# Kernel tuning notes

Hardware: AMD Instinct MI355X
Metric: run time of the kernel (lower is better)

Reference implementation:

```python
import jax, jax.numpy as jnp
import numpy as np
import math

B, T = 32768, 34
VOCAB = 14
SQRT_HD = math.sqrt(3.0)

def _pos_flat_index():
    # flatten (source, index) pairs into indices of a [14,3] table:
    # rows 0-9 = digit spiral enc, row 10 = z10_enc, rows 11-13 = special_enc
    flat = []
    for p in range(34):
        if p < 10:
            flat.append(p)
        elif p == 10:
            flat.append(11 + 0)
        elif p < 21:
            flat.append(p - 11)
        elif p == 21:
            flat.append(11 + 1)
        elif p < 33:
            z = p - 22
            flat.append(z if z < 10 else 10)
        else:
            flat.append(11 + 2)
    return np.array(flat, dtype=np.int32)

POS_FLAT = _pos_flat_index()

def setup_inputs() -> dict:
    key = jax.random.key(0)
    ks = jax.random.split(key, 12)
    r = lambda k, s: jax.random.normal(k, s, dtype=jnp.float32)
    return {
        'idx': jax.random.randint(ks[0], (B, T), 0, VOCAB, dtype=jnp.int64),
        'tok_emb': r(ks[1], (14, 3)),
        'pos_params': r(ks[2], (4,)),
        'z10_enc': r(ks[3], (1, 3)),
        'special_enc': r(ks[4], (3, 3)),
        'wq': r(ks[5], (3, 6)), 'wk': r(ks[6], (3, 6)), 'wv': r(ks[7], (3, 6)),
        'wo': r(ks[8], (6, 6)),
        'ln1_g': jnp.ones(6), 'ln1_b': jnp.zeros(6),
        'ln2_g': jnp.ones(6), 'ln2_b': jnp.zeros(6),
        'lnf_g': jnp.ones(6), 'lnf_b': jnp.zeros(6),
        'ffn_w1': r(ks[9], (6, 2)), 'ffn_b1': jnp.zeros(2),
        'ffn_w2': r(ks[10], (2, 6)), 'ffn_b2': jnp.zeros(6),
        'head_w': r(ks[11], (6, 3)),
    }

def _ln(x, g, b):
    mu = x.mean(-1, keepdims=True)
    var = ((x - mu) ** 2).mean(-1, keepdims=True)
    return (x - mu) * jax.lax.rsqrt(var + 1e-5) * g + b

def _forward(idx, tok_emb, pos_params, z10_enc, special_enc, wq, wk, wv, wo,
             ln1_g, ln1_b, ln2_g, ln2_b, lnf_g, lnf_b,
             ffn_w1, ffn_b1, ffn_w2, ffn_b2, head_w):
    amp, phase, slope, offset = pos_params[0], pos_params[1], pos_params[2], pos_params[3]
    i = jnp.arange(10, dtype=jnp.float32)
    ang = 2.0 * math.pi * i / 10.0 + phase
    digit = jnp.stack([amp * jnp.cos(ang), amp * jnp.sin(ang), slope * i + offset], -1)  # [10,3]
    table = jnp.concatenate([digit, z10_enc, special_enc], 0)  # [14,3]
    Tn = idx.shape[1]
    pos = table[POS_FLAT][:Tn]  # [T,3]
    tok = tok_emb[idx]  # [B,T,3]
    x = jnp.concatenate([tok, jnp.broadcast_to(pos, tok.shape)], -1)  # [B,T,6]
    h = _ln(x, ln1_g, ln1_b)
    h_tok, h_pos = h[..., :3], h[..., 3:]
    Bn = idx.shape[0]
    q = (h_pos @ wq).reshape(Bn, Tn, 2, 3)
    k = (h_pos @ wk).reshape(Bn, Tn, 2, 3)
    v = (h_tok @ wv).reshape(Bn, Tn, 2, 3)
    attn = jnp.einsum('bqhd,bkhd->bhqk', q, k) / SQRT_HD
    mask = jnp.tril(jnp.ones((Tn, Tn), bool))
    attn = jax.nn.softmax(jnp.where(mask, attn, -jnp.inf), axis=-1)
    o = jnp.einsum('bhqk,bkhd->bqhd', attn, v).reshape(Bn, Tn, 6)
    x = x + o @ wo
    h2 = _ln(x, ln2_g, ln2_b)
    x = x + (jax.nn.gelu(h2 @ ffn_w1 + ffn_b1, approximate=False) @ ffn_w2 + ffn_b2)
    x = _ln(x, lnf_g, lnf_b)
    return (x @ head_w) @ tok_emb.T  # [B,T,14]

def reference(idx, tok_emb, pos_params, z10_enc, special_enc, wq, wk, wv, wo,
              ln1_g, ln1_b, ln2_g, ln2_b, lnf_g, lnf_b,
              ffn_w1, ffn_b1, ffn_w2, ffn_b2, head_w):
    return _forward(idx, tok_emb, pos_params, z10_enc, special_enc, wq, wk, wv, wo,
                    ln1_g, ln1_b, ln2_g, ln2_b, lnf_g, lnf_b,
                    ffn_w1, ffn_b1, ffn_w2, ffn_b2, head_w)
```

## Files before the change

kernel.cpp:

```cpp
#include <hip/hip_runtime.h>
#include <math.h>

#define BT    34
#define TPR   17
#define RPB   15
#define BLOCK 256

typedef float v2f __attribute__((ext_vector_type(2)));
typedef float v4f __attribute__((ext_vector_type(4)));

#define QSCALE 0.83294037332470f

#if __has_builtin(__builtin_amdgcn_exp2f)
#define EXP2(x) __builtin_amdgcn_exp2f(x)
#else
#define EXP2(x) exp2f(x)
#endif

__device__ __forceinline__ void ln6n(const v2f* x, v2f* o) {
  v2f mu = (x[0]+x[1]+x[2]+x[3]+x[4]+x[5]) * (1.0f/6.0f);
  v2f v = (v2f){0.f, 0.f};
  #pragma unroll
  for (int c = 0; c < 6; ++c) { v2f d = x[c]-mu; v += d*d; }
  v2f inv = (v2f){ rsqrtf(v.x*(1.0f/6.0f) + 1e-5f),
                   rsqrtf(v.y*(1.0f/6.0f) + 1e-5f) };
  #pragma unroll
  for (int c = 0; c < 6; ++c) o[c] = (x[c]-mu)*inv;
}

__global__ __launch_bounds__(BLOCK, 6)
void addtrans_kernel(const int* __restrict__ idx,
                     const float* __restrict__ tok_emb,
                     const float* __restrict__ pos_params,
                     const float* __restrict__ z10_enc,
                     const float* __restrict__ special_enc,
                     const float* __restrict__ wq,
                     const float* __restrict__ wk,
                     const float* __restrict__ wv,
                     const float* __restrict__ wo,
                     const float* __restrict__ ln1_g, const float* __restrict__ ln1_b,
                     const float* __restrict__ ln2_g, const float* __restrict__ ln2_b,
                     const float* __restrict__ lnf_g, const float* __restrict__ lnf_b,
                     const float* __restrict__ ffn_w1, const float* __restrict__ ffn_b1,
                     const float* __restrict__ ffn_w2, const float* __restrict__ ffn_b2,
                     const float* __restrict__ head_w,
                     float* __restrict__ out, int B)
{
  __shared__ __align__(16) float s_mem[RPB*BT*12 + 180];
  __shared__ float s_te[42];
  __shared__ float s_pos[BT*3];
  __shared__ float s_wqf[18], s_wkf[18], s_wvf[18];
  __shared__ float s_qb[6], s_kb[6], s_vb[6];
  __shared__ float s_wo[36];
  __shared__ float s_w1f[12], s_fb1f[2];
  __shared__ float s_w2[12], s_fb2[6];
  __shared__ float s_hwf[18], s_yb[3];

  const int tid = threadIdx.x;
  const int b0  = blockIdx.x * RPB;

  if (tid < 42) s_te[tid] = tok_emb[tid];
  if (tid < 18) {
    const int r = tid / 6;
    s_wqf[tid] = wq[tid] * ln1_g[3+r];
    s_wkf[tid] = wk[tid] * ln1_g[3+r];
    s_wvf[tid] = wv[tid] * ln1_g[r];
    s_hwf[tid] = head_w[tid] * lnf_g[tid/3];
  }
  if (tid < 36) s_wo[tid] = wo[tid];
  if (tid < 12) { s_w1f[tid] = ffn_w1[tid] * ln2_g[tid>>1]; s_w2[tid] = ffn_w2[tid]; }
  if (tid < 6)  {
    s_qb[tid] = ln1_b[3]*wq[tid] + ln1_b[4]*wq[6+tid] + ln1_b[5]*wq[12+tid];
    s_kb[tid] = ln1_b[3]*wk[tid] + ln1_b[4]*wk[6+tid] + ln1_b[5]*wk[12+tid];
    s_vb[tid] = ln1_b[0]*wv[tid] + ln1_b[1]*wv[6+tid] + ln1_b[2]*wv[12+tid];
    s_fb2[tid] = ffn_b2[tid];
  }
  if (tid < 3) {
    float a = 0.f;
    #pragma unroll
    for (int c = 0; c < 6; ++c) a += lnf_b[c]*head_w[c*3+tid];
    s_yb[tid] = a;
  }
  if (tid < 2) {
    float a = ffn_b1[tid];
    #pragma unroll
    for (int d = 0; d < 6; ++d) a += ln2_b[d]*ffn_w1[d*2+tid];
    s_fb1f[tid] = a;
  }
  if (tid < BT) {
    int p = tid, f;
    if (p < 10) f = p;
    else if (p == 10) f = 11;
    else if (p < 21) f = p - 11;
    else if (p == 21) f = 12;
    else if (p < 33) { int z = p - 22; f = (z < 10) ? z : 10; }
    else f = 13;
    float e0, e1, e2;
    if (f < 10) {
      float amp = pos_params[0], ph = pos_params[1], sl = pos_params[2], of = pos_params[3];
      float ang = 0.62831853071795864769f * (float)f + ph;
      e0 = amp * cosf(ang); e1 = amp * sinf(ang); e2 = sl * (float)f + of;
    } else if (f == 10) { e0 = z10_enc[0]; e1 = z10_enc[1]; e2 = z10_enc[2]; }
    else { int u = f - 11; e0 = special_enc[u*3]; e1 = special_enc[u*3+1]; e2 = special_enc[u*3+2]; }
    s_pos[tid*3+0] = e0; s_pos[tid*3+1] = e1; s_pos[tid*3+2] = e2;
  }
  __syncthreads();

  const int row = tid % RPB;
  const int j   = tid / RPB;
  const int b   = b0 + row;
  const bool active = (j < TPR) && (b < B);

  v2f qpA[3], qpB[3];
  v2f x6[6];

  if (active) {
    const int tA = j, tB = j + TPR;
    const int vA = idx[b*BT + tA];
    const int vB = idx[b*BT + tB];
    #pragma unroll
    for (int c = 0; c < 3; ++c) {
      x6[c]   = (v2f){ s_te[vA*3+c],  s_te[vB*3+c]  };
      x6[3+c] = (v2f){ s_pos[tA*3+c], s_pos[tB*3+c] };
    }
    v2f h[6];
    ln6n(x6, h);
    v2f q6[6], k6[6], v6[6];
    #pragma unroll
    for (int c = 0; c < 6; ++c) {
      q6[c] = (v2f){s_qb[c], s_qb[c]} + h[3]*s_wqf[c] + h[4]*s_wqf[6+c] + h[5]*s_wqf[12+c];
      k6[c] = (v2f){s_kb[c], s_kb[c]} + h[3]*s_wkf[c] + h[4]*s_wkf[6+c] + h[5]*s_wkf[12+c];
      v6[c] = (v2f){s_vb[c], s_vb[c]} + h[0]*s_wvf[c] + h[1]*s_wvf[6+c] + h[2]*s_wvf[12+c];
    }
    #pragma unroll
    for (int d = 0; d < 3; ++d) {
      qpA[d] = (v2f){ q6[d].x, q6[3+d].x } * QSCALE;
      qpB[d] = (v2f){ q6[d].y, q6[3+d].y } * QSCALE;
    }
    v4f* pA = (v4f*)&s_mem[(tA*RPB + row)*12];
    pA[0] = (v4f){ k6[0].x, k6[3].x, k6[1].x, k6[4].x };
    pA[1] = (v4f){ k6[2].x, k6[5].x, v6[0].x, v6[3].x };
    pA[2] = (v4f){ v6[1].x, v6[4].x, v6[2].x, v6[5].x };
    v4f* pB = (v4f*)&s_mem[(tB*RPB + row)*12];
    pB[0] = (v4f){ k6[0].y, k6[3].y, k6[1].y, k6[4].y };
    pB[1] = (v4f){ k6[2].y, k6[5].y, v6[0].y, v6[3].y };
    pB[2] = (v4f){ v6[1].y, v6[4].y, v6[2].y, v6[5].y };
  }
  __syncthreads();

  v2f l0 = (v2f){0.f,0.f}, l1 = (v2f){0.f,0.f};
  v2f o0[3] = {(v2f){0.f,0.f},(v2f){0.f,0.f},(v2f){0.f,0.f}};
  v2f o1[3] = {(v2f){0.f,0.f},(v2f){0.f,0.f},(v2f){0.f,0.f}};
  if (active) {
    const float* kvbase = s_mem + row*12;
    v4f A  = ((const v4f*)kvbase)[0];
    v4f Bv = ((const v4f*)kvbase)[1];
    v4f C  = ((const v4f*)kvbase)[2];
    for (int k = 0; k <= j; ++k) {
      const v4f Ac = A, Bc = Bv, Cc = C;
      const v4f* nxt = (const v4f*)(kvbase + (k+1)*(RPB*12));
      A = nxt[0]; Bv = nxt[1]; C = nxt[2];
      v2f kA = (v2f){Ac.x, Ac.y}, kB = (v2f){Ac.z, Ac.w}, kC = (v2f){Bc.x, Bc.y};
      v2f vA = (v2f){Bc.z, Bc.w}, vB = (v2f){Cc.x, Cc.y}, vC = (v2f){Cc.z, Cc.w};
      v2f s0 = qpA[0]*kA + qpA[1]*kB + qpA[2]*kC;
      v2f p0 = (v2f){EXP2(s0.x), EXP2(s0.y)};
      l0 += p0; o0[0] += p0*vA; o0[1] += p0*vB; o0[2] += p0*vC;
      v2f s1 = qpB[0]*kA + qpB[1]*kB + qpB[2]*kC;
      v2f p1 = (v2f){EXP2(s1.x), EXP2(s1.y)};
      l1 += p1; o1[0] += p1*vA; o1[1] += p1*vB; o1[2] += p1*vC;
    }
    #pragma unroll 4
    for (int i = 1; i <= TPR; ++i) {
      const int k = j + i;
      const v4f Ac = A, Bc = Bv, Cc = C;
      const v4f* nxt = (const v4f*)(kvbase + (k+1)*(RPB*12));
      A = nxt[0]; Bv = nxt[1]; C = nxt[2];
      v2f kA = (v2f){Ac.x, Ac.y}, kB = (v2f){Ac.z, Ac.w}, kC = (v2f){Bc.x, Bc.y};
      v2f vA = (v2f){Bc.z, Bc.w}, vB = (v2f){Cc.x, Cc.y}, vC = (v2f){Cc.z, Cc.w};
      v2f s1 = qpB[0]*kA + qpB[1]*kB + qpB[2]*kC;
      v2f p1 = (v2f){EXP2(s1.x), EXP2(s1.y)};
      l1 += p1; o1[0] += p1*vA; o1[1] += p1*vB; o1[2] += p1*vC;
    }
  }

  if (active) {
    const float rA0 = __builtin_amdgcn_rcpf(l0.x);
    const float rA1 = __builtin_amdgcn_rcpf(l0.y);
    const float rB0 = __builtin_amdgcn_rcpf(l1.x);
    const float rB1 = __builtin_amdgcn_rcpf(l1.y);
    v2f a6[6];
    a6[0] = (v2f){ o0[0].x*rA0, o1[0].x*rB0 };
    a6[1] = (v2f){ o0[1].x*rA0, o1[1].x*rB0 };
    a6[2] = (v2f){ o0[2].x*rA0, o1[2].x*rB0 };
    a6[3] = (v2f){ o0[0].y*rA1, o1[0].y*rB1 };
    a6[4] = (v2f){ o0[1].y*rA1, o1[1].y*rB1 };
    a6[5] = (v2f){ o0[2].y*rA1, o1[2].y*rB1 };
    v2f xn[6];
    #pragma unroll
    for (int c = 0; c < 6; ++c) {
      xn[c] = x6[c]
            + a6[0]*s_wo[c]    + a6[1]*s_wo[6+c]  + a6[2]*s_wo[12+c]
            + a6[3]*s_wo[18+c] + a6[4]*s_wo[24+c] + a6[5]*s_wo[30+c];
    }
    v2f t2[6];
    ln6n(xn, t2);
    v2f a0 = (v2f){s_fb1f[0], s_fb1f[0]};
    v2f a1 = (v2f){s_fb1f[1], s_fb1f[1]};
    #pragma unroll
    for (int d = 0; d < 6; ++d) { a0 += t2[d]*s_w1f[d*2]; a1 += t2[d]*s_w1f[d*2+1]; }
    const float KIS2 = 0.70710678118654752440f;
    v2f g0 = (v2f){ 0.5f*a0.x*(1.0f + erff(a0.x*KIS2)),
                    0.5f*a0.y*(1.0f + erff(a0.y*KIS2)) };
    v2f g1 = (v2f){ 0.5f*a1.x*(1.0f + erff(a1.x*KIS2)),
                    0.5f*a1.y*(1.0f + erff(a1.y*KIS2)) };
    #pragma unroll
    for (int c = 0; c < 6; ++c) xn[c] += g0*s_w2[c] + g1*s_w2[6+c] + s_fb2[c];
    v2f tf[6];
    ln6n(xn, tf);
    v2f y0 = (v2f){s_yb[0], s_yb[0]};
    v2f y1 = (v2f){s_yb[1], s_yb[1]};
    v2f y2 = (v2f){s_yb[2], s_yb[2]};
    #pragma unroll
    for (int c = 0; c < 6; ++c) {
      y0 += tf[c]*s_hwf[c*3+0]; y1 += tf[c]*s_hwf[c*3+1]; y2 += tf[c]*s_hwf[c*3+2];
    }
    float* oA = out + ((size_t)b * BT + j) * 14;
    float* oB = oA + TPR * 14;
    #pragma unroll
    for (int u = 0; u < 7; ++u) {
      const int c0 = 2*u, c1 = 2*u+1;
      v2f lg0 = y0*s_te[c0*3+0] + y1*s_te[c0*3+1] + y2*s_te[c0*3+2];
      v2f lg1 = y0*s_te[c1*3+0] + y1*s_te[c1*3+1] + y2*s_te[c1*3+2];
      *reinterpret_cast<v2f*>(oA + 2*u) = (v2f){ lg0.x, lg1.x };
      *reinterpret_cast<v2f*>(oB + 2*u) = (v2f){ lg0.y, lg1.y };
    }
  }
}

extern "C" void kernel_launch(void* const* d_in, const int* in_sizes, int n_in,
                              void* d_out, int out_size, void* d_ws, size_t ws_size,
                              hipStream_t stream) {
  const int B = in_sizes[0] / BT;
  const int grid = (B + RPB - 1) / RPB;
  addtrans_kernel<<<grid, BLOCK, 0, stream>>>(
      (const int*)d_in[0],   (const float*)d_in[1], (const float*)d_in[2],
      (const float*)d_in[3], (const float*)d_in[4], (const float*)d_in[5],
      (const float*)d_in[6], (const float*)d_in[7], (const float*)d_in[8],
      (const float*)d_in[9], (const float*)d_in[10], (const float*)d_in[11],
      (const float*)d_in[12], (const float*)d_in[13], (const float*)d_in[14],
      (const float*)d_in[15], (const float*)d_in[16], (const float*)d_in[17],
      (const float*)d_in[18], (const float*)d_in[19],
      (float*)d_out, B);
}
```

Before: 140.5 us.

## Stage idx loads and logits through shared memory for coalesced nontemporal I/O

The kernel now copies each block's idx rows into shared memory with a strided, coalesced loop instead of per-thread scattered loads. Logits are written into an enlarged shared buffer and then streamed to global memory as contiguous v4f nontemporal stores, replacing the previous strided 8-byte stores. The aim is better coalescing on the output write, which dominates traffic at 14 floats per token. In exchange it uses more LDS, adds two block barriers, and lowers the launch-bounds occupancy hint from 6 to 5.

```diff
diff --git a/kernel.cpp b/kernel.cpp
--- a/kernel.cpp
+++ b/kernel.cpp
@@ -28,7 +28,7 @@
   for (int c = 0; c < 6; ++c) o[c] = (x[c]-mu)*inv;
 }
 
-__global__ __launch_bounds__(BLOCK, 6)
+__global__ __launch_bounds__(BLOCK, 5)
 void addtrans_kernel(const int* __restrict__ idx,
                      const float* __restrict__ tok_emb,
                      const float* __restrict__ pos_params,
@@ -46,7 +46,8 @@
                      const float* __restrict__ head_w,
                      float* __restrict__ out, int B)
 {
-  __shared__ __align__(16) float s_mem[RPB*BT*12 + 180];
+  __shared__ __align__(16) float s_mem[RPB*BT*14];
+  __shared__ int   s_idx[RPB*BT];
   __shared__ float s_te[42];
   __shared__ float s_pos[BT*3];
   __shared__ float s_wqf[18], s_wkf[18], s_wvf[18];
@@ -86,6 +87,11 @@
     #pragma unroll
     for (int d = 0; d < 6; ++d) a += ln2_b[d]*ffn_w1[d*2+tid];
     s_fb1f[tid] = a;
+  }
+  {
+    int nr = B - b0; if (nr > RPB) nr = RPB;
+    const int tot = nr * BT;
+    for (int i = tid; i < tot; i += BLOCK) s_idx[i] = idx[b0*BT + i];
   }
   if (tid < BT) {
     int p = tid, f;
@@ -116,8 +122,8 @@
 
   if (active) {
     const int tA = j, tB = j + TPR;
-    const int vA = idx[b*BT + tA];
-    const int vB = idx[b*BT + tB];
+    const int vA = s_idx[row*BT + tA];
+    const int vB = s_idx[row*BT + tB];
     #pragma unroll
     for (int c = 0; c < 3; ++c) {
       x6[c]   = (v2f){ s_te[vA*3+c],  s_te[vB*3+c]  };
@@ -182,6 +188,7 @@
       l1 += p1; o1[0] += p1*vA; o1[1] += p1*vB; o1[2] += p1*vC;
     }
   }
+  __syncthreads();
 
   if (active) {
     const float rA0 = __builtin_amdgcn_rcpf(l0.x);
@@ -224,15 +231,27 @@
     for (int c = 0; c < 6; ++c) {
       y0 += tf[c]*s_hwf[c*3+0]; y1 += tf[c]*s_hwf[c*3+1]; y2 += tf[c]*s_hwf[c*3+2];
     }
-    float* oA = out + ((size_t)b * BT + j) * 14;
-    float* oB = oA + TPR * 14;
+    v2f* lpA = (v2f*)&s_mem[(row*BT + j      )*14];
+    v2f* lpB = (v2f*)&s_mem[(row*BT + j + TPR)*14];
     #pragma unroll
     for (int u = 0; u < 7; ++u) {
       const int c0 = 2*u, c1 = 2*u+1;
       v2f lg0 = y0*s_te[c0*3+0] + y1*s_te[c0*3+1] + y2*s_te[c0*3+2];
       v2f lg1 = y0*s_te[c1*3+0] + y1*s_te[c1*3+1] + y2*s_te[c1*3+2];
-      *reinterpret_cast<v2f*>(oA + 2*u) = (v2f){ lg0.x, lg1.x };
-      *reinterpret_cast<v2f*>(oB + 2*u) = (v2f){ lg0.y, lg1.y };
+      lpA[u] = (v2f){ lg0.x, lg1.x };
+      lpB[u] = (v2f){ lg0.y, lg1.y };
+    }
+  }
+  __syncthreads();
+
+  {
+    int nrows = B - b0; if (nrows > RPB) nrows = RPB;
+    if (nrows > 0) {
+      const int n4 = nrows * (BT*14/4);
+      v4f* dst = reinterpret_cast<v4f*>(out + (size_t)b0 * (BT*14));
+      const v4f* src = reinterpret_cast<const v4f*>(s_mem);
+      for (int i = tid; i < n4; i += BLOCK)
+        __builtin_nontemporal_store(src[i], dst + i);
     }
   }
 }
```

Result: faster. 133.9 us (-4.7%).
